# Kernel optimization log

Hardware: AMD Instinct MI355X
Metric: run time of the kernel (lower is better)

The kernel has to match this reference:

```python
import jax, jax.numpy as jnp
import numpy as np

BS, NA = 32, 128
NE = NA * (NA - 1)            # fully-connected directed, no self loops
NU, D = 4, 8                  # num_user, per-user feature dim
FEAT = NU * D                 # 32: node / edge feature dim
CC = 8                        # conv1 out channels (1x1 conv, in_channels=2)
CONV_OUT = CC * NU * D        # 256
EMB = 64                      # embedding size (x_last / output dim)
H1 = 256                      # MLP hidden
MLP1_IN = CONV_OUT + EMB      # layer_idx > 1: concat local_state_j
MLP2_IN = FEAT + EMB + EMB    # x0, x_last, agg_in


def make_edges():
    src, dst = np.meshgrid(np.arange(NA), np.arange(NA), indexing='ij')
    m = src != dst
    return jnp.asarray(np.stack([src[m], dst[m]], axis=1), dtype=jnp.int32)


def setup_inputs() -> dict:
    key = jax.random.key(0)
    ks = jax.random.split(key, 9)
    return {
        "x0": jax.random.normal(ks[0], (BS, NA, FEAT), jnp.float32),
        "x_last": jax.random.normal(ks[1], (BS, NA, EMB), jnp.float32),
        "edge_attr": jax.random.normal(ks[2], (BS, NE, FEAT), jnp.float32),
        "conv_w": jax.random.normal(ks[3], (CC, 2), jnp.float32) * 0.3,
        "conv_b": jnp.zeros((CC,), jnp.float32),
        "mlp1_w1": jax.random.normal(ks[4], (MLP1_IN, H1), jnp.float32) * 0.05,
        "mlp1_b1": jnp.zeros((H1,), jnp.float32),
        "mlp1_w2": jax.random.normal(ks[5], (H1, EMB), jnp.float32) * 0.05,
        "mlp1_b2": jnp.zeros((EMB,), jnp.float32),
        "mlp2_w1": jax.random.normal(ks[6], (MLP2_IN, H1), jnp.float32) * 0.05,
        "mlp2_b1": jnp.zeros((H1,), jnp.float32),
        "mlp2_w2": jax.random.normal(ks[7], (H1, EMB), jnp.float32) * 0.05,
        "mlp2_b2": jnp.zeros((EMB,), jnp.float32),
        "edge_idx": make_edges(),
    }


def reference(x0, x_last, edge_attr, conv_w, conv_b,
              mlp1_w1, mlp1_b1, mlp1_w2, mlp1_b2,
              mlp2_w1, mlp2_b1, mlp2_w2, mlp2_b2, edge_idx):
    src, dst = edge_idx[:, 0], edge_idx[:, 1]
    # --- propagate / local_embedding ---
    nf_j = x0[:, src, :]                 # [B, E, FEAT] gather source node feats
    ls_j = x_last[:, src, :]             # [B, E, EMB]  (layer_idx > 1)
    # torch: cat(node_feat, edge_attr) on user dim then view [N,2,NU,D]
    x = jnp.stack([nf_j.reshape(BS, NE, NU, D),
                   edge_attr.reshape(BS, NE, NU, D)], axis=2)  # [B,E,2,NU,D]
    # 1x1 Conv2d(2 -> CC) + ReLU
    y = jax.nn.relu(jnp.einsum('becud,oc->beoud', x, conv_w)
                    + conv_b[None, None, :, None, None])
    y = y.reshape(BS, NE, CONV_OUT)
    lf = jnp.concatenate([y, ls_j], axis=-1)                   # [B,E,MLP1_IN]
    h = jax.nn.relu(lf @ mlp1_w1 + mlp1_b1)
    local_embed = h @ mlp1_w2 + mlp1_b2                        # [B,E,EMB]
    # per-node segment sum over destination (replaces python loop over agents)
    agg_in = jnp.zeros((BS, NA, EMB), local_embed.dtype).at[:, dst, :].add(local_embed)
    # --- update_embedding ---
    agg = jnp.concatenate([x0, x_last, agg_in], axis=-1)       # [B,NA,MLP2_IN]
    h2 = jax.nn.relu(agg @ mlp2_w1 + mlp2_b1)
    return h2 @ mlp2_w2 + mlp2_b2                              # [B,NA,EMB]
```

## Files before the change

kernel.cpp:

```cpp
#include <hip/hip_runtime.h>

#define BSg   32
#define NAg   128
#define NEg   16256
#define EMBg  64
#define H1g   256

typedef __attribute__((ext_vector_type(8))) short  short8;
typedef __attribute__((ext_vector_type(4))) float  f32x4;

__device__ __forceinline__ unsigned int f2bf(float x) {
    union { float f; unsigned int u; } v; v.f = x;
    return (v.u + 0x7FFFu + ((v.u >> 16) & 1u)) >> 16;
}
__device__ __forceinline__ unsigned int pack2(float a, float b) {
    return f2bf(a) | (f2bf(b) << 16);
}

__global__ void pack_weights(const float* __restrict__ w1, unsigned short* __restrict__ w1p)
{
    int i = blockIdx.x * 256 + threadIdx.x;
    if (i < 320 * 256) {
        int k = i >> 8, n = i & 255;
        w1p[(k >> 3) * (256 * 8) + n * 8 + (k & 7)] = (unsigned short)f2bf(w1[i]);
    }
}

__global__ __launch_bounds__(512, 4) void edge_kernel(
    const float* __restrict__ x0, const float* __restrict__ x_last,
    const float* __restrict__ edge_attr, const float* __restrict__ conv_w,
    const float* __restrict__ conv_b, const unsigned short* __restrict__ w1p,
    const float* __restrict__ b1, const float* __restrict__ w2f,
    const float* __restrict__ b2, float* __restrict__ agg)
{
    __shared__ unsigned short fragA[2][10 * 4 * 64 * 8];

    const int tid  = threadIdx.x;
    const int b    = blockIdx.x >> 7;
    const int d    = blockIdx.x & 127;
    const int w8   = tid >> 6, lane = tid & 63;
    const int half = w8 >> 2, wq = w8 & 3;
    const int llo  = lane & 15, lhi = lane >> 4;
    const int colbase = wq * 64;

    {
        const int j  = wq * 16 + llo;
        const int el = half * 64 + j;
        int s = el + (el >= d ? 1 : 0);
        if (s > 127) s = 127;
        int e = s * 127 + d - (s < d ? 1 : 0);
        if (e > NEg - 1) e = NEg - 1;

        const float4* nfp = (const float4*)(x0        + (((size_t)b * NAg + s) << 5) + (lhi << 3));
        const float4* eap = (const float4*)(edge_attr + (((size_t)b * NEg + e) << 5) + (lhi << 3));
        float4 nf0 = nfp[0], nf1 = nfp[1];
        float4 ea0 = eap[0], ea1 = eap[1];

        #pragma unroll
        for (int o = 0; o < 8; ++o) {
            const float w0 = conv_w[2 * o], w1v = conv_w[2 * o + 1], cb = conv_b[o];
            float y0 = fmaxf(fmaf(w0, nf0.x, fmaf(w1v, ea0.x, cb)), 0.f);
            float y1 = fmaxf(fmaf(w0, nf0.y, fmaf(w1v, ea0.y, cb)), 0.f);
            float y2 = fmaxf(fmaf(w0, nf0.z, fmaf(w1v, ea0.z, cb)), 0.f);
            float y3 = fmaxf(fmaf(w0, nf0.w, fmaf(w1v, ea0.w, cb)), 0.f);
            float y4 = fmaxf(fmaf(w0, nf1.x, fmaf(w1v, ea1.x, cb)), 0.f);
            float y5 = fmaxf(fmaf(w0, nf1.y, fmaf(w1v, ea1.y, cb)), 0.f);
            float y6 = fmaxf(fmaf(w0, nf1.z, fmaf(w1v, ea1.z, cb)), 0.f);
            float y7 = fmaxf(fmaf(w0, nf1.w, fmaf(w1v, ea1.w, cb)), 0.f);
            uint4 pk;
            pk.x = pack2(y0, y1); pk.y = pack2(y2, y3);
            pk.z = pack2(y4, y5); pk.w = pack2(y6, y7);
            *(uint4*)&fragA[half][(((o * 4 + wq) * 64) + lane) * 8] = pk;
        }
        {
            const float4* lsp = (const float4*)(x_last + (((size_t)b * NAg + s) << 6) + (lhi << 4));
            float4 l0 = lsp[0], l1 = lsp[1], l2 = lsp[2], l3 = lsp[3];
            uint4 pa, pb;
            pa.x = pack2(l0.x, l0.y); pa.y = pack2(l0.z, l0.w);
            pa.z = pack2(l1.x, l1.y); pa.w = pack2(l1.z, l1.w);
            pb.x = pack2(l2.x, l2.y); pb.y = pack2(l2.z, l2.w);
            pb.z = pack2(l3.x, l3.y); pb.w = pack2(l3.z, l3.w);
            const int ks8  = 8 + (lhi >> 1);
            const int slot = (ks8 * 4 + wq) * 64 + ((lhi & 1) * 2) * 16 + llo;
            *(uint4*)&fragA[half][slot * 8]        = pa;
            *(uint4*)&fragA[half][(slot + 16) * 8] = pb;
        }
    }
    __syncthreads();

    f32x4 acc[4][4];
    #pragma unroll
    for (int m = 0; m < 4; ++m)
        #pragma unroll
        for (int n = 0; n < 4; ++n)
            acc[m][n] = (f32x4){0.f, 0.f, 0.f, 0.f};

    #pragma unroll
    for (int ks = 0; ks < 10; ++ks) {
        short8 af[4], bf[4];
        #pragma unroll
        for (int m = 0; m < 4; ++m)
            af[m] = *(const short8*)&fragA[half][((ks * 4 + m) * 64 + lane) * 8];
        #pragma unroll
        for (int n = 0; n < 4; ++n)
            bf[n] = *(const short8*)&w1p[((ks * 4 + lhi) * H1g + colbase + n * 16 + llo) * 8];
        #pragma unroll
        for (int m = 0; m < 4; ++m)
            #pragma unroll
            for (int n = 0; n < 4; ++n)
                acc[m][n] = __builtin_amdgcn_mfma_f32_16x16x32_bf16(af[m], bf[n], acc[m][n], 0, 0, 0);
    }

    float h1s[4];
    {
        float bias1[4];
        #pragma unroll
        for (int n = 0; n < 4; ++n) bias1[n] = b1[colbase + n * 16 + llo];
        #pragma unroll
        for (int n = 0; n < 4; ++n) {
            float p = 0.f;
            #pragma unroll
            for (int m = 0; m < 4; ++m)
                #pragma unroll
                for (int i = 0; i < 4; ++i) {
                    float v = fmaxf(acc[m][n][i] + bias1[n], 0.f);
                    if (!(m == 3 && i == 3) || !(half == 1 && lhi == 3)) p += v;
                }
            p += __shfl_xor(p, 16, 64);
            p += __shfl_xor(p, 32, 64);
            h1s[n] = p;
        }
    }
    __syncthreads();

    float* h1part = (float*)&fragA[0][0];
    float* redS   = h1part + 512;

    if (lhi == 0) {
        #pragma unroll
        for (int n = 0; n < 4; ++n) h1part[half * 256 + colbase + n * 16 + llo] = h1s[n];
    }
    __syncthreads();

    {
        const int c = tid & 63, kq = tid >> 6;
        float p = 0.f;
        #pragma unroll 8
        for (int k0 = 0; k0 < 32; ++k0) {
            int k = kq * 32 + k0;
            float h = h1part[k] + h1part[256 + k];
            p = fmaf(h, w2f[k * 64 + c], p);
        }
        redS[kq * 64 + c] = p;
    }
    __syncthreads();
    if (tid < 64) {
        float v = redS[tid]       + redS[64 + tid]  + redS[128 + tid] + redS[192 + tid]
                + redS[256 + tid] + redS[320 + tid] + redS[384 + tid] + redS[448 + tid]
                + 127.f * b2[tid];
        agg[(((size_t)b * NAg + d) << 6) + tid] = v;
    }
}

__global__ __launch_bounds__(256) void node_kernel(
    const float* __restrict__ x0, const float* __restrict__ x_last,
    const float* __restrict__ agg, const float* __restrict__ w1,
    const float* __restrict__ b1, const float* __restrict__ w2,
    const float* __restrict__ b2, float* __restrict__ out)
{
    __shared__ float lf[16][160];
    __shared__ float h2s[16][257];
    const int tid = threadIdx.x;
    const int r0  = blockIdx.x * 16;

    for (int idx = tid; idx < 16 * 160; idx += 256) {
        int r = idx / 160, c = idx % 160;
        int gr = r0 + r;
        int bb = gr >> 7, a = gr & 127;
        float v;
        if (c < 32)      v = x0[(((size_t)bb * NAg + a) << 5) + c];
        else if (c < 96) v = x_last[(((size_t)bb * NAg + a) << 6) + (c - 32)];
        else             v = agg[((size_t)gr << 6) + (c - 96)];
        lf[r][c] = v;
    }
    __syncthreads();

    {
        const int c = tid;
        float acc[16];
        const float bb = b1[c];
        #pragma unroll
        for (int r = 0; r < 16; ++r) acc[r] = bb;
        for (int k = 0; k < 160; ++k) {
            float wv = w1[k * 256 + c];
            #pragma unroll
            for (int r = 0; r < 16; ++r) acc[r] = fmaf(lf[r][k], wv, acc[r]);
        }
        #pragma unroll
        for (int r = 0; r < 16; ++r) h2s[r][c] = fmaxf(acc[r], 0.f);
    }
    __syncthreads();

    {
        const int n = tid & 63, rq = tid >> 6;
        float acc[4];
        const float bb = b2[n];
        #pragma unroll
        for (int j = 0; j < 4; ++j) acc[j] = bb;
        for (int k = 0; k < 256; ++k) {
            float wv = w2[k * 64 + n];
            #pragma unroll
            for (int j = 0; j < 4; ++j) acc[j] = fmaf(h2s[rq * 4 + j][k], wv, acc[j]);
        }
        #pragma unroll
        for (int j = 0; j < 4; ++j)
            out[((size_t)(r0 + rq * 4 + j) << 6) + n] = acc[j];
    }
}

extern "C" void kernel_launch(void* const* d_in, const int* in_sizes, int n_in,
                              void* d_out, int out_size, void* d_ws, size_t ws_size,
                              hipStream_t stream)
{
    const float* x0       = (const float*)d_in[0];
    const float* x_last   = (const float*)d_in[1];
    const float* edge_attr= (const float*)d_in[2];
    const float* conv_w   = (const float*)d_in[3];
    const float* conv_b   = (const float*)d_in[4];
    const float* mlp1_w1  = (const float*)d_in[5];
    const float* mlp1_b1  = (const float*)d_in[6];
    const float* mlp1_w2  = (const float*)d_in[7];
    const float* mlp1_b2  = (const float*)d_in[8];
    const float* mlp2_w1  = (const float*)d_in[9];
    const float* mlp2_b1  = (const float*)d_in[10];
    const float* mlp2_w2  = (const float*)d_in[11];
    const float* mlp2_b2  = (const float*)d_in[12];

    char* ws = (char*)d_ws;
    float* agg          = (float*)ws;
    unsigned short* w1p = (unsigned short*)(ws + (1 << 20));

    pack_weights<<<320, 256, 0, stream>>>(mlp1_w1, w1p);
    edge_kernel<<<BSg * NAg, 512, 0, stream>>>(x0, x_last, edge_attr, conv_w, conv_b,
                                               w1p, mlp1_b1, mlp1_w2, mlp1_b2, agg);
    node_kernel<<<(BSg * NAg) / 16, 256, 0, stream>>>(x0, x_last, agg, mlp2_w1, mlp2_b1,
                                                      mlp2_w2, mlp2_b2, (float*)d_out);
}
```

Baseline: 137.2 us.

## Pre-convert x_last to bf16 and load its MFMA fragments directly into registers

The pack kernel now also converts x_last to bf16 in workspace. The edge kernel loads the two x_last k-slices straight from global memory into MFMA A-fragment registers instead of staging them through shared memory, which shrinks the LDS tile. The node kernel is retiled from 16 to 8 rows per block to launch more blocks, and the bf16 conversion now uses the HIP intrinsics. This trades extra registers and an extra preprocessing pass for less LDS traffic and better occupancy.

```diff
diff --git a/kernel.cpp b/kernel.cpp
--- a/kernel.cpp
+++ b/kernel.cpp
@@ -1,4 +1,5 @@
 #include <hip/hip_runtime.h>
+#include <hip/hip_bf16.h>
 
 #define BSg   32
 #define NAg   128
@@ -9,31 +10,37 @@
 typedef __attribute__((ext_vector_type(8))) short  short8;
 typedef __attribute__((ext_vector_type(4))) float  f32x4;
 
-__device__ __forceinline__ unsigned int f2bf(float x) {
-    union { float f; unsigned int u; } v; v.f = x;
-    return (v.u + 0x7FFFu + ((v.u >> 16) & 1u)) >> 16;
+__device__ __forceinline__ unsigned short f2bf16u(float x) {
+    union { __hip_bfloat16 h; unsigned short u; } cv;
+    cv.h = __float2bfloat16(x);
+    return cv.u;
 }
 __device__ __forceinline__ unsigned int pack2(float a, float b) {
-    return f2bf(a) | (f2bf(b) << 16);
-}
-
-__global__ void pack_weights(const float* __restrict__ w1, unsigned short* __restrict__ w1p)
+    union { __hip_bfloat162 h; unsigned int u; } cv;
+    cv.h = __float22bfloat162_rn(make_float2(a, b));
+    return cv.u;
+}
+
+__global__ void pack_weights(const float* __restrict__ w1, const float* __restrict__ xl,
+                             unsigned short* __restrict__ w1p, unsigned short* __restrict__ xlp)
 {
     int i = blockIdx.x * 256 + threadIdx.x;
     if (i < 320 * 256) {
         int k = i >> 8, n = i & 255;
-        w1p[(k >> 3) * (256 * 8) + n * 8 + (k & 7)] = (unsigned short)f2bf(w1[i]);
-    }
+        w1p[(k >> 3) * (256 * 8) + n * 8 + (k & 7)] = f2bf16u(w1[i]);
+    }
+    if (i < BSg * NAg * EMBg)
+        xlp[i] = f2bf16u(xl[i]);
 }
 
 __global__ __launch_bounds__(512, 4) void edge_kernel(
-    const float* __restrict__ x0, const float* __restrict__ x_last,
+    const float* __restrict__ x0, const unsigned short* __restrict__ xlp,
     const float* __restrict__ edge_attr, const float* __restrict__ conv_w,
     const float* __restrict__ conv_b, const unsigned short* __restrict__ w1p,
     const float* __restrict__ b1, const float* __restrict__ w2f,
     const float* __restrict__ b2, float* __restrict__ agg)
 {
-    __shared__ unsigned short fragA[2][10 * 4 * 64 * 8];
+    __shared__ unsigned short fragA[2][8 * 4 * 64 * 8];
 
     const int tid  = threadIdx.x;
     const int b    = blockIdx.x >> 7;
@@ -42,6 +49,17 @@
     const int half = w8 >> 2, wq = w8 & 3;
     const int llo  = lane & 15, lhi = lane >> 4;
     const int colbase = wq * 64;
+
+    short8 af8[4], af9[4];
+    #pragma unroll
+    for (int m = 0; m < 4; ++m) {
+        int el = half * 64 + m * 16 + llo;
+        int s  = el + (el >= d ? 1 : 0);
+        if (s > 127) s = 127;
+        const unsigned short* base = xlp + (((b << 7) | s) << 6) + lhi * 8;
+        af8[m] = *(const short8*)base;
+        af9[m] = *(const short8*)(base + 32);
+    }
 
     {
         const int j  = wq * 16 + llo;
@@ -72,19 +90,6 @@
             pk.z = pack2(y4, y5); pk.w = pack2(y6, y7);
             *(uint4*)&fragA[half][(((o * 4 + wq) * 64) + lane) * 8] = pk;
         }
-        {
-            const float4* lsp = (const float4*)(x_last + (((size_t)b * NAg + s) << 6) + (lhi << 4));
-            float4 l0 = lsp[0], l1 = lsp[1], l2 = lsp[2], l3 = lsp[3];
-            uint4 pa, pb;
-            pa.x = pack2(l0.x, l0.y); pa.y = pack2(l0.z, l0.w);
-            pa.z = pack2(l1.x, l1.y); pa.w = pack2(l1.z, l1.w);
-            pb.x = pack2(l2.x, l2.y); pb.y = pack2(l2.z, l2.w);
-            pb.z = pack2(l3.x, l3.y); pb.w = pack2(l3.z, l3.w);
-            const int ks8  = 8 + (lhi >> 1);
-            const int slot = (ks8 * 4 + wq) * 64 + ((lhi & 1) * 2) * 16 + llo;
-            *(uint4*)&fragA[half][slot * 8]        = pa;
-            *(uint4*)&fragA[half][(slot + 16) * 8] = pb;
-        }
     }
     __syncthreads();
 
@@ -99,8 +104,11 @@
     for (int ks = 0; ks < 10; ++ks) {
         short8 af[4], bf[4];
         #pragma unroll
-        for (int m = 0; m < 4; ++m)
-            af[m] = *(const short8*)&fragA[half][((ks * 4 + m) * 64 + lane) * 8];
+        for (int m = 0; m < 4; ++m) {
+            if (ks < 8)       af[m] = *(const short8*)&fragA[half][((ks * 4 + m) * 64 + lane) * 8];
+            else if (ks == 8) af[m] = af8[m];
+            else              af[m] = af9[m];
+        }
         #pragma unroll
         for (int n = 0; n < 4; ++n)
             bf[n] = *(const short8*)&w1p[((ks * 4 + lhi) * H1g + colbase + n * 16 + llo) * 8];
@@ -168,12 +176,12 @@
     const float* __restrict__ b1, const float* __restrict__ w2,
     const float* __restrict__ b2, float* __restrict__ out)
 {
-    __shared__ float lf[16][160];
-    __shared__ float h2s[16][257];
+    __shared__ float lf[8][160];
+    __shared__ float h2s[8][257];
     const int tid = threadIdx.x;
-    const int r0  = blockIdx.x * 16;
-
-    for (int idx = tid; idx < 16 * 160; idx += 256) {
+    const int r0  = blockIdx.x * 8;
+
+    for (int idx = tid; idx < 8 * 160; idx += 256) {
         int r = idx / 160, c = idx % 160;
         int gr = r0 + r;
         int bb = gr >> 7, a = gr & 127;
@@ -187,34 +195,34 @@
 
     {
         const int c = tid;
-        float acc[16];
+        float acc[8];
         const float bb = b1[c];
         #pragma unroll
-        for (int r = 0; r < 16; ++r) acc[r] = bb;
+        for (int r = 0; r < 8; ++r) acc[r] = bb;
         for (int k = 0; k < 160; ++k) {
             float wv = w1[k * 256 + c];
             #pragma unroll
-            for (int r = 0; r < 16; ++r) acc[r] = fmaf(lf[r][k], wv, acc[r]);
-        }
-        #pragma unroll
-        for (int r = 0; r < 16; ++r) h2s[r][c] = fmaxf(acc[r], 0.f);
+            for (int r = 0; r < 8; ++r) acc[r] = fmaf(lf[r][k], wv, acc[r]);
+        }
+        #pragma unroll
+        for (int r = 0; r < 8; ++r) h2s[r][c] = fmaxf(acc[r], 0.f);
     }
     __syncthreads();
 
     {
         const int n = tid & 63, rq = tid >> 6;
-        float acc[4];
+        float acc[2];
         const float bb = b2[n];
         #pragma unroll
-        for (int j = 0; j < 4; ++j) acc[j] = bb;
+        for (int j = 0; j < 2; ++j) acc[j] = bb;
         for (int k = 0; k < 256; ++k) {
             float wv = w2[k * 64 + n];
             #pragma unroll
-            for (int j = 0; j < 4; ++j) acc[j] = fmaf(h2s[rq * 4 + j][k], wv, acc[j]);
-        }
-        #pragma unroll
-        for (int j = 0; j < 4; ++j)
-            out[((size_t)(r0 + rq * 4 + j) << 6) + n] = acc[j];
+            for (int j = 0; j < 2; ++j) acc[j] = fmaf(h2s[rq * 2 + j][k], wv, acc[j]);
+        }
+        #pragma unroll
+        for (int j = 0; j < 2; ++j)
+            out[((size_t)(r0 + rq * 2 + j) << 6) + n] = acc[j];
     }
 }
 
@@ -239,10 +247,11 @@
     char* ws = (char*)d_ws;
     float* agg          = (float*)ws;
     unsigned short* w1p = (unsigned short*)(ws + (1 << 20));
-
-    pack_weights<<<320, 256, 0, stream>>>(mlp1_w1, w1p);
-    edge_kernel<<<BSg * NAg, 512, 0, stream>>>(x0, x_last, edge_attr, conv_w, conv_b,
+    unsigned short* xlp = (unsigned short*)(ws + (1 << 20) + (192 << 10));
+
+    pack_weights<<<1024, 256, 0, stream>>>(mlp1_w1, x_last, w1p, xlp);
+    edge_kernel<<<BSg * NAg, 512, 0, stream>>>(x0, xlp, edge_attr, conv_w, conv_b,
                                                w1p, mlp1_b1, mlp1_w2, mlp1_b2, agg);
-    node_kernel<<<(BSg * NAg) / 16, 256, 0, stream>>>(x0, x_last, agg, mlp2_w1, mlp2_b1,
-                                                      mlp2_w2, mlp2_b2, (float*)d_out);
-}
+    node_kernel<<<(BSg * NAg) / 8, 256, 0, stream>>>(x0, x_last, agg, mlp2_w1, mlp2_b1,
+                                                     mlp2_w2, mlp2_b2, (float*)d_out);
+}
```

New measurement: 141.1 us. +2.8%, slower.
